# Kernel optimization log

Hardware: AMD Instinct MI355X
Metric: run time of the kernel (lower is better)

## Reference

```python
import jax, jax.numpy as jnp
import numpy as np

B, C_IN, C_OUT, V, K = 4, 64, 64, 163842, 7  # level-7 icosphere: 10*4^7+2 vertices

def setup_inputs() -> dict:
    key = jax.random.key(0)
    k1, k2, k3, k4, k5 = jax.random.split(key, 5)
    x = jax.random.normal(k1, (B, C_IN, V), dtype=jnp.float32)
    index = jax.random.randint(k2, (V, K), 0, V, dtype=jnp.int32)
    itp_mat = jax.random.normal(k3, (V, K, K), dtype=jnp.float32) * 0.2
    conv_w = jax.random.normal(k4, (C_OUT, C_IN, 1, K), dtype=jnp.float32) * 0.05
    conv_b = jax.random.normal(k5, (C_OUT,), dtype=jnp.float32) * 0.05
    return {"x": x, "index": index, "itp_mat": itp_mat, "conv_w": conv_w, "conv_b": conv_b}

def reference(x, index, itp_mat, conv_w, conv_b):
    # interpolate(): permute(2,0,1) -> [V,B,C]; t[index] -> [V,K,B,C];
    # train_select_index == arange(V) (select_index=None, stride=1) -> identity;
    # permute(2,3,0,1) -> [B,C,V,K]. Equivalent single gather:
    g = x[:, :, index]                                   # [B, C, V, K]
    # unsqueeze(-2) @ itp_mat[V,K,K], squeeze(-2): per-vertex interpolation matmul
    itp = jnp.einsum('bcvk,vkj->bcvj', g, itp_mat)       # [B, C, V, K]
    # Conv2d(C_in, C_out, (1, K)) over [B,C,V,K] -> [B,C_out,V,1], then squeeze(-1)
    out = jnp.einsum('bcvj,ocj->bov', itp, conv_w[:, :, 0, :]) + conv_b[None, :, None]
    return out                                            # [B, C_out, V]
```

## Files before the change

### kernel.cpp

```cpp
#include <hip/hip_runtime.h>

#define BN 4
#define CN 64
#define ON 64
#define VN 163842
#define KN 7
#define JN 7
#define CJ 448
#define GROUP 8
#define NGROUPS ((VN + GROUP - 1) / GROUP)
#define GRID 512
#define VT_CHUNKS ((VN + 63) / 64)

__launch_bounds__(256, 4)
__global__ void transpose_kernel(const float* __restrict__ x, float* __restrict__ xT) {
    __shared__ float tile[64][65];
    const int bid   = blockIdx.x;
    const int b     = bid / VT_CHUNKS;
    const int vbase = (bid % VT_CHUNKS) * 64;
    const int t     = threadIdx.x;
    const int vl    = t & 63;
    const int cr    = t >> 6;

    if (vbase + vl < VN) {
        #pragma unroll
        for (int i = 0; i < 16; ++i) {
            const int c = cr * 16 + i;
            tile[c][vl] = x[((size_t)b * CN + c) * VN + vbase + vl];
        }
    }
    __syncthreads();
    #pragma unroll
    for (int i = 0; i < 16; ++i) {
        const int vr = cr * 16 + i;
        const int v  = vbase + vr;
        if (v < VN)
            xT[((size_t)b * VN + v) * CN + (t & 63)] = tile[t & 63][vr];
    }
}

__launch_bounds__(256, 2)
__global__ void sphere_conv_xt(const float* __restrict__ xT,
                               const int* __restrict__ index,
                               const float* __restrict__ itp,
                               const float* __restrict__ w,
                               const float* __restrict__ bias,
                               float* __restrict__ out) {
    __shared__ float Tl[GROUP][CJ][4];
    float* red = &Tl[0][0][0];

    const int t  = threadIdx.x;
    const int o  = t & 63;
    const int cq = t >> 6;

    float wreg[112];
    {
        const float4* wp = reinterpret_cast<const float4*>(w + o * CJ + cq * 112);
        #pragma unroll
        for (int i = 0; i < 28; ++i) {
            float4 f = wp[i];
            wreg[i*4+0] = f.x; wreg[i*4+1] = f.y; wreg[i*4+2] = f.z; wreg[i*4+3] = f.w;
        }
    }

    const int cA = t & 63;
    const int bA = t >> 6;

    for (int g = blockIdx.x; g < NGROUPS; g += gridDim.x) {
        const int vbase = g * GROUP;

        for (int vi = 0; vi < GROUP; ++vi) {
            const int v = min(vbase + vi, VN - 1);
            const int*   ip = index + v * KN;
            const float* mp = itp   + v * KN * JN;
            float xv[KN];
            #pragma unroll
            for (int k = 0; k < KN; ++k) {
                const int ik = ip[k];
                xv[k] = xT[((size_t)bA * VN + ik) * CN + cA];
            }
            #pragma unroll
            for (int j = 0; j < JN; ++j) {
                float tj = 0.f;
                #pragma unroll
                for (int k = 0; k < KN; ++k) tj = fmaf(xv[k], mp[k * JN + j], tj);
                Tl[vi][cA * JN + j][bA] = tj;
            }
        }
        __syncthreads();

        float acc[GROUP][4];
        #pragma unroll
        for (int vi = 0; vi < GROUP; ++vi) {
            acc[vi][0] = 0.f; acc[vi][1] = 0.f; acc[vi][2] = 0.f; acc[vi][3] = 0.f;
        }
        #pragma unroll
        for (int e = 0; e < 112; ++e) {
            const int cj = cq * 112 + e;
            const float wv = wreg[e];
            #pragma unroll
            for (int vi = 0; vi < GROUP; ++vi) {
                const float4 tv = *reinterpret_cast<const float4*>(&Tl[vi][cj][0]);
                acc[vi][0] = fmaf(tv.x, wv, acc[vi][0]);
                acc[vi][1] = fmaf(tv.y, wv, acc[vi][1]);
                acc[vi][2] = fmaf(tv.z, wv, acc[vi][2]);
                acc[vi][3] = fmaf(tv.w, wv, acc[vi][3]);
            }
        }
        __syncthreads();

        #pragma unroll
        for (int vi = 0; vi < GROUP; ++vi) {
            float4 f;
            f.x = acc[vi][0]; f.y = acc[vi][1]; f.z = acc[vi][2]; f.w = acc[vi][3];
            *reinterpret_cast<float4*>(&red[(cq * 64 + o) * 36 + vi * 4]) = f;
        }
        __syncthreads();

        const int vloc = t & 7;
        #pragma unroll
        for (int p = 0; p < 8; ++p) {
            const int bo = (t >> 3) + p * 32;
            const int oo = bo & 63;
            const int bb = bo >> 6;
            float s = bias[oo];
            #pragma unroll
            for (int q = 0; q < 4; ++q)
                s += red[(q * 64 + oo) * 36 + vloc * 4 + bb];
            const int v = vbase + vloc;
            if (v < VN) out[(size_t)bo * VN + v] = s;
        }
        __syncthreads();
    }
}

__launch_bounds__(256, 2)
__global__ void sphere_conv_fallback(const float* __restrict__ x,
                                     const int* __restrict__ index,
                                     const float* __restrict__ itp,
                                     const float* __restrict__ w,
                                     const float* __restrict__ bias,
                                     float* __restrict__ out) {
    __shared__ float Tl[GROUP][CJ][4];
    float* red = &Tl[0][0][0];
    const int t  = threadIdx.x;
    const int o  = t & 63;
    const int cq = t >> 6;
    float wreg[112];
    {
        const float4* wp = reinterpret_cast<const float4*>(w + o * CJ + cq * 112);
        #pragma unroll
        for (int i = 0; i < 28; ++i) {
            float4 f = wp[i];
            wreg[i*4+0] = f.x; wreg[i*4+1] = f.y; wreg[i*4+2] = f.z; wreg[i*4+3] = f.w;
        }
    }
    const int cA = t & 63;
    const int bA = t >> 6;
    for (int g = blockIdx.x; g < NGROUPS; g += gridDim.x) {
        const int vbase = g * GROUP;
        for (int vi = 0; vi < GROUP; ++vi) {
            const int v = min(vbase + vi, VN - 1);
            const int*   ip = index + v * KN;
            const float* mp = itp   + v * KN * JN;
            float xv[KN];
            #pragma unroll
            for (int k = 0; k < KN; ++k) xv[k] = x[(size_t)(bA * CN + cA) * VN + ip[k]];
            #pragma unroll
            for (int j = 0; j < JN; ++j) {
                float tj = 0.f;
                #pragma unroll
                for (int k = 0; k < KN; ++k) tj = fmaf(xv[k], mp[k * JN + j], tj);
                Tl[vi][cA * JN + j][bA] = tj;
            }
        }
        __syncthreads();
        float acc[GROUP][4];
        #pragma unroll
        for (int vi = 0; vi < GROUP; ++vi) {
            acc[vi][0] = 0.f; acc[vi][1] = 0.f; acc[vi][2] = 0.f; acc[vi][3] = 0.f;
        }
        #pragma unroll
        for (int e = 0; e < 112; ++e) {
            const int cj = cq * 112 + e;
            const float wv = wreg[e];
            #pragma unroll
            for (int vi = 0; vi < GROUP; ++vi) {
                const float4 tv = *reinterpret_cast<const float4*>(&Tl[vi][cj][0]);
                acc[vi][0] = fmaf(tv.x, wv, acc[vi][0]);
                acc[vi][1] = fmaf(tv.y, wv, acc[vi][1]);
                acc[vi][2] = fmaf(tv.z, wv, acc[vi][2]);
                acc[vi][3] = fmaf(tv.w, wv, acc[vi][3]);
            }
        }
        __syncthreads();
        #pragma unroll
        for (int vi = 0; vi < GROUP; ++vi) {
            float4 f;
            f.x = acc[vi][0]; f.y = acc[vi][1]; f.z = acc[vi][2]; f.w = acc[vi][3];
            *reinterpret_cast<float4*>(&red[(cq * 64 + o) * 36 + vi * 4]) = f;
        }
        __syncthreads();
        const int vloc = t & 7;
        #pragma unroll
        for (int p = 0; p < 8; ++p) {
            const int bo = (t >> 3) + p * 32;
            const int oo = bo & 63;
            const int bb = bo >> 6;
            float s = bias[oo];
            #pragma unroll
            for (int q = 0; q < 4; ++q)
                s += red[(q * 64 + oo) * 36 + vloc * 4 + bb];
            const int v = vbase + vloc;
            if (v < VN) out[(size_t)bo * VN + v] = s;
        }
        __syncthreads();
    }
}

extern "C" void kernel_launch(void* const* d_in, const int* in_sizes, int n_in,
                              void* d_out, int out_size, void* d_ws, size_t ws_size,
                              hipStream_t stream) {
    const float* x     = (const float*)d_in[0];
    const int*   index = (const int*)  d_in[1];
    const float* itp   = (const float*)d_in[2];
    const float* w     = (const float*)d_in[3];
    const float* bias  = (const float*)d_in[4];
    float*       out   = (float*)d_out;

    const size_t xt_bytes = (size_t)BN * VN * CN * sizeof(float);

    if (ws_size >= xt_bytes) {
        float* xT = (float*)d_ws;
        transpose_kernel<<<dim3(BN * VT_CHUNKS), dim3(256), 0, stream>>>(x, xT);
        sphere_conv_xt<<<dim3(GRID), dim3(256), 0, stream>>>(xT, index, itp, w, bias, out);
    } else {
        sphere_conv_fallback<<<dim3(GRID), dim3(256), 0, stream>>>(x, index, itp, w, bias, out);
    }
}
```

Before: 2.772 ms.

## Restructure sphere conv to 512-thread blocks with swizzled LDS and halved weight registers

```diff
diff --git a/kernel.cpp b/kernel.cpp
--- a/kernel.cpp
+++ b/kernel.cpp
@@ -7,9 +7,10 @@
 #define KN 7
 #define JN 7
 #define CJ 448
-#define GROUP 8
-#define NGROUPS ((VN + GROUP - 1) / GROUP)
+#define GROUP 4
+#define NG ((VN + GROUP - 1) / GROUP)
 #define GRID 512
+#define GPB ((NG + GRID - 1) / GRID)
 #define VT_CHUNKS ((VN + 63) / 64)
 
 __launch_bounds__(256, 4)
@@ -39,52 +40,55 @@
     }
 }
 
-__launch_bounds__(256, 2)
-__global__ void sphere_conv_xt(const float* __restrict__ xT,
+__launch_bounds__(512, 4)
+__global__ void sphere_conv_v3(const float* __restrict__ xT,
                                const int* __restrict__ index,
                                const float* __restrict__ itp,
                                const float* __restrict__ w,
                                const float* __restrict__ bias,
                                float* __restrict__ out) {
-    __shared__ float Tl[GROUP][CJ][4];
-    float* red = &Tl[0][0][0];
-
-    const int t  = threadIdx.x;
-    const int o  = t & 63;
-    const int cq = t >> 6;
-
-    float wreg[112];
-    {
-        const float4* wp = reinterpret_cast<const float4*>(w + o * CJ + cq * 112);
-        #pragma unroll
-        for (int i = 0; i < 28; ++i) {
-            float4 f = wp[i];
-            wreg[i*4+0] = f.x; wreg[i*4+1] = f.y; wreg[i*4+2] = f.z; wreg[i*4+3] = f.w;
-        }
-    }
-
-    const int cA = t & 63;
-    const int bA = t >> 6;
-
-    for (int g = blockIdx.x; g < NGROUPS; g += gridDim.x) {
+    __shared__ float Tl[GROUP * 1792];
+    __shared__ float red[8 * 64 * 16];
+
+    const int t    = threadIdx.x;
+    const int lane = t & 63;
+    const int wv   = t >> 6;
+
+    const int o  = lane;
+    const int cq = wv;
+
+    float wreg[56];
+    #pragma unroll
+    for (int e = 0; e < 56; ++e)
+        wreg[e] = w[o * CJ + (8 * (e & 7) + cq) * JN + (e >> 3)];
+
+    const int bA = wv & 3;
+    const int vh = wv >> 2;
+
+    const int bid = blockIdx.x;
+    for (int g0 = 0; g0 < GPB; ++g0) {
+        const int g = bid * GPB + g0;
+        if (g >= NG) break;
         const int vbase = g * GROUP;
 
-        for (int vi = 0; vi < GROUP; ++vi) {
-            const int v = min(vbase + vi, VN - 1);
+        #pragma unroll
+        for (int vi2 = 0; vi2 < 2; ++vi2) {
+            const int vi = vh * 2 + vi2;
+            const int v  = min(vbase + vi, VN - 1);
             const int*   ip = index + v * KN;
-            const float* mp = itp   + v * KN * JN;
+            const float* mp = itp   + v * (KN * JN);
             float xv[KN];
             #pragma unroll
             for (int k = 0; k < KN; ++k) {
-                const int ik = ip[k];
-                xv[k] = xT[((size_t)bA * VN + ik) * CN + cA];
+                const unsigned ik = (unsigned)ip[k];
+                xv[k] = xT[(unsigned)(bA * VN + ik) * CN + lane];
             }
             #pragma unroll
             for (int j = 0; j < JN; ++j) {
                 float tj = 0.f;
                 #pragma unroll
                 for (int k = 0; k < KN; ++k) tj = fmaf(xv[k], mp[k * JN + j], tj);
-                Tl[vi][cA * JN + j][bA] = tj;
+                Tl[vi * 1792 + j * 256 + lane * 4 + (bA ^ ((lane >> 3) & 3))] = tj;
             }
         }
         __syncthreads();
@@ -95,16 +99,17 @@
             acc[vi][0] = 0.f; acc[vi][1] = 0.f; acc[vi][2] = 0.f; acc[vi][3] = 0.f;
         }
         #pragma unroll
-        for (int e = 0; e < 112; ++e) {
-            const int cj = cq * 112 + e;
-            const float wv = wreg[e];
+        for (int e = 0; e < 56; ++e) {
+            const int   base = (e >> 3) * 256 + 32 * (e & 7) + 4 * cq;
+            const float we   = wreg[e];
+            const int   s    = e & 3;
             #pragma unroll
             for (int vi = 0; vi < GROUP; ++vi) {
-                const float4 tv = *reinterpret_cast<const float4*>(&Tl[vi][cj][0]);
-                acc[vi][0] = fmaf(tv.x, wv, acc[vi][0]);
-                acc[vi][1] = fmaf(tv.y, wv, acc[vi][1]);
-                acc[vi][2] = fmaf(tv.z, wv, acc[vi][2]);
-                acc[vi][3] = fmaf(tv.w, wv, acc[vi][3]);
+                const float4 tv = *reinterpret_cast<const float4*>(&Tl[vi * 1792 + base]);
+                acc[vi][0 ^ s] = fmaf(tv.x, we, acc[vi][0 ^ s]);
+                acc[vi][1 ^ s] = fmaf(tv.y, we, acc[vi][1 ^ s]);
+                acc[vi][2 ^ s] = fmaf(tv.z, we, acc[vi][2 ^ s]);
+                acc[vi][3 ^ s] = fmaf(tv.w, we, acc[vi][3 ^ s]);
             }
         }
         __syncthreads();
@@ -113,65 +118,69 @@
         for (int vi = 0; vi < GROUP; ++vi) {
             float4 f;
             f.x = acc[vi][0]; f.y = acc[vi][1]; f.z = acc[vi][2]; f.w = acc[vi][3];
-            *reinterpret_cast<float4*>(&red[(cq * 64 + o) * 36 + vi * 4]) = f;
-        }
-        __syncthreads();
-
-        const int vloc = t & 7;
-        #pragma unroll
-        for (int p = 0; p < 8; ++p) {
-            const int bo = (t >> 3) + p * 32;
-            const int oo = bo & 63;
-            const int bb = bo >> 6;
+            *reinterpret_cast<float4*>(&red[(cq * 64 + o) * 16 + (vi ^ (o & 3)) * 4]) = f;
+        }
+        __syncthreads();
+
+        #pragma unroll
+        for (int p = 0; p < 2; ++p) {
+            const int item = t + p * 512;
+            const int vloc = item & 3;
+            const int bo   = item >> 2;
+            const int oo   = bo & 63;
+            const int bb   = bo >> 6;
             float s = bias[oo];
             #pragma unroll
-            for (int q = 0; q < 4; ++q)
-                s += red[(q * 64 + oo) * 36 + vloc * 4 + bb];
-            const int v = vbase + vloc;
-            if (v < VN) out[(size_t)bo * VN + v] = s;
-        }
-        __syncthreads();
-    }
-}
-
-__launch_bounds__(256, 2)
-__global__ void sphere_conv_fallback(const float* __restrict__ x,
-                                     const int* __restrict__ index,
-                                     const float* __restrict__ itp,
-                                     const float* __restrict__ w,
-                                     const float* __restrict__ bias,
-                                     float* __restrict__ out) {
-    __shared__ float Tl[GROUP][CJ][4];
-    float* red = &Tl[0][0][0];
-    const int t  = threadIdx.x;
-    const int o  = t & 63;
-    const int cq = t >> 6;
-    float wreg[112];
-    {
-        const float4* wp = reinterpret_cast<const float4*>(w + o * CJ + cq * 112);
-        #pragma unroll
-        for (int i = 0; i < 28; ++i) {
-            float4 f = wp[i];
-            wreg[i*4+0] = f.x; wreg[i*4+1] = f.y; wreg[i*4+2] = f.z; wreg[i*4+3] = f.w;
-        }
-    }
-    const int cA = t & 63;
-    const int bA = t >> 6;
-    for (int g = blockIdx.x; g < NGROUPS; g += gridDim.x) {
+            for (int q = 0; q < 8; ++q)
+                s += red[(q * 64 + oo) * 16 + (vloc ^ (oo & 3)) * 4 + bb];
+            const int vv = vbase + vloc;
+            if (vv < VN) out[(unsigned)bo * VN + vv] = s;
+        }
+        __syncthreads();
+    }
+}
+
+__launch_bounds__(512, 4)
+__global__ void sphere_conv_fb(const float* __restrict__ x,
+                               const int* __restrict__ index,
+                               const float* __restrict__ itp,
+                               const float* __restrict__ w,
+                               const float* __restrict__ bias,
+                               float* __restrict__ out) {
+    __shared__ float Tl[GROUP * 1792];
+    __shared__ float red[8 * 64 * 16];
+    const int t    = threadIdx.x;
+    const int lane = t & 63;
+    const int wv   = t >> 6;
+    const int o  = lane;
+    const int cq = wv;
+    float wreg[56];
+    #pragma unroll
+    for (int e = 0; e < 56; ++e)
+        wreg[e] = w[o * CJ + (8 * (e & 7) + cq) * JN + (e >> 3)];
+    const int bA = wv & 3;
+    const int vh = wv >> 2;
+    const int bid = blockIdx.x;
+    for (int g0 = 0; g0 < GPB; ++g0) {
+        const int g = bid * GPB + g0;
+        if (g >= NG) break;
         const int vbase = g * GROUP;
-        for (int vi = 0; vi < GROUP; ++vi) {
-            const int v = min(vbase + vi, VN - 1);
+        #pragma unroll
+        for (int vi2 = 0; vi2 < 2; ++vi2) {
+            const int vi = vh * 2 + vi2;
+            const int v  = min(vbase + vi, VN - 1);
             const int*   ip = index + v * KN;
-            const float* mp = itp   + v * KN * JN;
+            const float* mp = itp   + v * (KN * JN);
             float xv[KN];
             #pragma unroll
-            for (int k = 0; k < KN; ++k) xv[k] = x[(size_t)(bA * CN + cA) * VN + ip[k]];
+            for (int k = 0; k < KN; ++k)
+                xv[k] = x[(size_t)(bA * CN + lane) * VN + ip[k]];
             #pragma unroll
             for (int j = 0; j < JN; ++j) {
                 float tj = 0.f;
                 #pragma unroll
                 for (int k = 0; k < KN; ++k) tj = fmaf(xv[k], mp[k * JN + j], tj);
-                Tl[vi][cA * JN + j][bA] = tj;
+                Tl[vi * 1792 + j * 256 + lane * 4 + (bA ^ ((lane >> 3) & 3))] = tj;
             }
         }
         __syncthreads();
@@ -181,16 +190,17 @@
             acc[vi][0] = 0.f; acc[vi][1] = 0.f; acc[vi][2] = 0.f; acc[vi][3] = 0.f;
         }
         #pragma unroll
-        for (int e = 0; e < 112; ++e) {
-            const int cj = cq * 112 + e;
-            const float wv = wreg[e];
+        for (int e = 0; e < 56; ++e) {
+            const int   base = (e >> 3) * 256 + 32 * (e & 7) + 4 * cq;
+            const float we   = wreg[e];
+            const int   s    = e & 3;
             #pragma unroll
             for (int vi = 0; vi < GROUP; ++vi) {
-                const float4 tv = *reinterpret_cast<const float4*>(&Tl[vi][cj][0]);
-                acc[vi][0] = fmaf(tv.x, wv, acc[vi][0]);
-                acc[vi][1] = fmaf(tv.y, wv, acc[vi][1]);
-                acc[vi][2] = fmaf(tv.z, wv, acc[vi][2]);
-                acc[vi][3] = fmaf(tv.w, wv, acc[vi][3]);
+                const float4 tv = *reinterpret_cast<const float4*>(&Tl[vi * 1792 + base]);
+                acc[vi][0 ^ s] = fmaf(tv.x, we, acc[vi][0 ^ s]);
+                acc[vi][1 ^ s] = fmaf(tv.y, we, acc[vi][1 ^ s]);
+                acc[vi][2 ^ s] = fmaf(tv.z, we, acc[vi][2 ^ s]);
+                acc[vi][3 ^ s] = fmaf(tv.w, we, acc[vi][3 ^ s]);
             }
         }
         __syncthreads();
@@ -198,21 +208,22 @@
         for (int vi = 0; vi < GROUP; ++vi) {
             float4 f;
             f.x = acc[vi][0]; f.y = acc[vi][1]; f.z = acc[vi][2]; f.w = acc[vi][3];
-            *reinterpret_cast<float4*>(&red[(cq * 64 + o) * 36 + vi * 4]) = f;
-        }
-        __syncthreads();
-        const int vloc = t & 7;
-        #pragma unroll
-        for (int p = 0; p < 8; ++p) {
-            const int bo = (t >> 3) + p * 32;
-            const int oo = bo & 63;
-            const int bb = bo >> 6;
+            *reinterpret_cast<float4*>(&red[(cq * 64 + o) * 16 + (vi ^ (o & 3)) * 4]) = f;
+        }
+        __syncthreads();
+        #pragma unroll
+        for (int p = 0; p < 2; ++p) {
+            const int item = t + p * 512;
+            const int vloc = item & 3;
+            const int bo   = item >> 2;
+            const int oo   = bo & 63;
+            const int bb   = bo >> 6;
             float s = bias[oo];
             #pragma unroll
-            for (int q = 0; q < 4; ++q)
-                s += red[(q * 64 + oo) * 36 + vloc * 4 + bb];
-            const int v = vbase + vloc;
-            if (v < VN) out[(size_t)bo * VN + v] = s;
+            for (int q = 0; q < 8; ++q)
+                s += red[(q * 64 + oo) * 16 + (vloc ^ (oo & 3)) * 4 + bb];
+            const int vv = vbase + vloc;
+            if (vv < VN) out[(unsigned)bo * VN + vv] = s;
         }
         __syncthreads();
     }
@@ -233,8 +244,8 @@
     if (ws_size >= xt_bytes) {
         float* xT = (float*)d_ws;
         transpose_kernel<<<dim3(BN * VT_CHUNKS), dim3(256), 0, stream>>>(x, xT);
-        sphere_conv_xt<<<dim3(GRID), dim3(256), 0, stream>>>(xT, index, itp, w, bias, out);
+        sphere_conv_v3<<<dim3(GRID), dim3(512), 0, stream>>>(xT, index, itp, w, bias, out);
     } else {
-        sphere_conv_fallback<<<dim3(GRID), dim3(256), 0, stream>>>(x, index, itp, w, bias, out);
-    }
-}
+        sphere_conv_fb<<<dim3(GRID), dim3(512), 0, stream>>>(x, index, itp, w, bias, out);
+    }
+}
```

Result: slower. 3.381 ms (+22.0%).
